# Optimization experiments

Measured on AMD Instinct MI355X. Metric: run time of the kernel, lower is better.

The kernel has to match this reference:

```python
import jax, jax.numpy as jnp
import numpy as np

C = 256  # image_channels == mask_channels == output_channels

def setup_inputs() -> dict:
    key = jax.random.key(0)
    ks = jax.random.split(key, 10)
    B, H, W = 16, 48, 48
    s = 0.02
    return {
        "image_feat": jax.random.normal(ks[0], (B, C, H, W), jnp.float32),
        "mask_feat": jax.random.normal(ks[1], (B, C, H, W), jnp.float32),
        "Wq": jax.random.normal(ks[2], (C, C), jnp.float32) * s,
        "bq": jnp.zeros((C,), jnp.float32),
        "Wk": jax.random.normal(ks[3], (C, C), jnp.float32) * s,
        "bk": jnp.zeros((C,), jnp.float32),
        "Wv": jax.random.normal(ks[4], (C, C), jnp.float32) * s,
        "bv": jnp.zeros((C,), jnp.float32),
        "Wo": jax.random.normal(ks[5], (C, C), jnp.float32) * s,
        "bo": jnp.zeros((C,), jnp.float32),
    }

def reference(image_feat, mask_feat, Wq, bq, Wk, bk, Wv, bv, Wo, bo):
    B, Cc, H, W = image_feat.shape
    N = H * W
    img = image_feat.reshape(B, Cc, N)   # [B, C, N]
    msk = mask_feat.reshape(B, Cc, N)
    # 1x1 convs == per-pixel linear over channels
    q = jnp.einsum('oc,bcn->bon', Wq, msk) + bq[None, :, None]
    k = jnp.einsum('oc,bcn->bon', Wk, img) + bk[None, :, None]
    v = jnp.einsum('oc,bcn->bon', Wv, img) + bv[None, :, None]
    scale = Cc ** (-0.5)
    # attn[b, n, m] = <q[:, n], k[:, m]>
    attn = jnp.einsum('bcn,bcm->bnm', q, k) * scale
    attn = jax.nn.softmax(attn, axis=-1)
    # attended[b, c, n] = sum_m v[b, c, m] * attn[b, n, m]
    av = jnp.einsum('bcm,bnm->bcn', v, attn)
    out = jnp.einsum('oc,bcn->bon', Wo, av) + bo[None, :, None]
    return image_feat + out.reshape(B, Cc, H, W)
```

## Files before the change

### kernel.cpp

```cpp
#include <hip/hip_runtime.h>

#define NBATCH 16
#define CCH 256
#define NTOK 2304

typedef __attribute__((ext_vector_type(8))) short bf16x8;
typedef __attribute__((ext_vector_type(4))) short bf16x4v;
typedef __attribute__((ext_vector_type(4))) float f32x4;

__device__ __forceinline__ short f2bf(float x){
  unsigned u = __builtin_bit_cast(unsigned, x);
  u = u + 0x7FFFu + ((u >> 16) & 1u);
  return (short)(u >> 16);
}
__device__ __forceinline__ float bf2f(short h){
  unsigned u = ((unsigned)(unsigned short)h) << 16;
  return __builtin_bit_cast(float, u);
}

__device__ __forceinline__ void gld_lds16(const short* g, short* l){
  __builtin_amdgcn_global_load_lds((const __attribute__((address_space(1))) void*)g,
                                   (__attribute__((address_space(3))) void*)l, 16, 0, 0);
}

__global__ __launch_bounds__(256) void cw_kernel(const float* __restrict__ Wq, const float* __restrict__ Wk,
                                                 const float* __restrict__ Wv, const float* __restrict__ Wo,
                                                 short* __restrict__ out){
  int idx = blockIdx.x * 256 + threadIdx.x;
  int which = idx >> 14;
  int off = idx & 16383;
  const float* src = which==0 ? Wq : which==1 ? Wk : which==2 ? Wv : Wo;
  float4 v = ((const float4*)src)[off];
  bf16x4v pk = { f2bf(v.x), f2bf(v.y), f2bf(v.z), f2bf(v.w) };
  *(bf16x4v*)(out + ((size_t)which << 16) + ((size_t)off << 2)) = pk;
}

__global__ __launch_bounds__(256) void prep_kernel(const float* __restrict__ img, const float* __restrict__ msk,
                                                   short* __restrict__ imgT, short* __restrict__ mskT){
  int zz = blockIdx.z; int b = zz >> 1; int which = zz & 1;
  const float* src = (which ? msk : img) + (size_t)b * CCH * NTOK;
  short* dst = (which ? mskT : imgT) + (size_t)b * NTOK * CCH;
  int n0 = blockIdx.x * 64, c0 = blockIdx.y * 64;
  __shared__ __align__(16) short tile[64][72];
  int tid = threadIdx.x;
  int r = tid >> 2, g = tid & 3;
  const float* p = src + (size_t)(c0 + r) * NTOK + n0 + 16 * g;
  #pragma unroll
  for (int q4 = 0; q4 < 4; q4++){
    float4 v = *(const float4*)(p + 4 * q4);
    tile[16*g + 4*q4 + 0][r] = f2bf(v.x);
    tile[16*g + 4*q4 + 1][r] = f2bf(v.y);
    tile[16*g + 4*q4 + 2][r] = f2bf(v.z);
    tile[16*g + 4*q4 + 3][r] = f2bf(v.w);
  }
  __syncthreads();
  short* qp = dst + (size_t)(n0 + r) * CCH + c0 + 16 * g;
  *(bf16x8*)qp = *(const bf16x8*)&tile[r][16*g];
  *(bf16x8*)(qp + 8) = *(const bf16x8*)&tile[r][16*g + 8];
}

__device__ __forceinline__ void gemm128(const short* __restrict__ Ablk, const short* __restrict__ Bblk,
                                        short* As, short* Bs, f32x4 (&acc)[4][4]){
  const int tid = threadIdx.x;
  const int l = tid & 63, w = tid >> 6;
  const int l15 = l & 15, lhi = l >> 4;
  const int wi = w >> 1, wj = w & 1;
  const int srow = tid >> 3, scs = tid & 7;
  const f32x4 z4 = {0.f, 0.f, 0.f, 0.f};
  #pragma unroll
  for (int mt = 0; mt < 4; mt++)
    #pragma unroll
    for (int nt = 0; nt < 4; nt++) acc[mt][nt] = z4;

  #pragma unroll 1
  for (int kt = 0; kt < 4; kt++){
    const int k0 = kt * 64;
    bf16x8 ra[4], rb[4];
    #pragma unroll
    for (int p = 0; p < 4; p++){
      const int row = p * 32 + srow;
      ra[p] = *(const bf16x8*)(Ablk + (size_t)row * CCH + k0 + 8 * scs);
      rb[p] = *(const bf16x8*)(Bblk + (size_t)row * CCH + k0 + 8 * scs);
    }
    __syncthreads();
    #pragma unroll
    for (int p = 0; p < 4; p++){
      const int row = p * 32 + srow;
      const int sw = (scs ^ (row & 7)) << 3;
      *(bf16x8*)(As + row * 64 + sw) = ra[p];
      *(bf16x8*)(Bs + row * 64 + sw) = rb[p];
    }
    __syncthreads();
    #pragma unroll
    for (int kk = 0; kk < 2; kk++){
      bf16x8 afr[4], bfr[4];
      #pragma unroll
      for (int mt = 0; mt < 4; mt++){
        const int row = 64 * wi + 16 * mt + l15;
        const int ch = 4 * kk + lhi;
        afr[mt] = *(const bf16x8*)(As + row * 64 + ((ch ^ (row & 7)) << 3));
      }
      #pragma unroll
      for (int nt = 0; nt < 4; nt++){
        const int row = 64 * wj + 16 * nt + l15;
        const int ch = 4 * kk + lhi;
        bfr[nt] = *(const bf16x8*)(Bs + row * 64 + ((ch ^ (row & 7)) << 3));
      }
      #pragma unroll
      for (int mt = 0; mt < 4; mt++)
        #pragma unroll
        for (int nt = 0; nt < 4; nt++)
          acc[mt][nt] = __builtin_amdgcn_mfma_f32_16x16x32_bf16(afr[mt], bfr[nt], acc[mt][nt], 0, 0, 0);
    }
  }
}

__global__ __launch_bounds__(256) void proj_kernel(const short* __restrict__ imgT, const short* __restrict__ mskT,
                                                   const short* __restrict__ Wb,
                                                   const float* __restrict__ bq, const float* __restrict__ bk,
                                                   const float* __restrict__ bv,
                                                   short* __restrict__ Qt, short* __restrict__ Kt,
                                                   short* __restrict__ Vn){
  __shared__ __align__(16) short As[128 * 64];
  __shared__ __align__(16) short Bs[128 * 64];
  const int b = blockIdx.z, which = blockIdx.y, bx = blockIdx.x;
  const size_t nbT = (size_t)b * NTOK * CCH;
  const short* Ablk; const short* Bblk; short* outp; const float* bias;
  int ti, tj, ldout; bool biasRow; float scl;
  if (which == 0){
    ti = bx >> 1; tj = bx & 1;
    Ablk = mskT + nbT + (size_t)ti * 128 * CCH;
    Bblk = Wb + (size_t)tj * 128 * CCH;
    outp = Qt + nbT; bias = bq; ldout = CCH; biasRow = false;
    scl = 0.0625f * 1.44269504088896f;
  } else if (which == 1){
    ti = bx >> 1; tj = bx & 1;
    Ablk = imgT + nbT + (size_t)ti * 128 * CCH;
    Bblk = Wb + 65536 + (size_t)tj * 128 * CCH;
    outp = Kt + nbT; bias = bk; ldout = CCH; biasRow = false; scl = 1.0f;
  } else {
    ti = bx / 18; tj = bx % 18;
    Ablk = Wb + 2 * 65536 + (size_t)ti * 128 * CCH;
    Bblk = imgT + nbT + (size_t)tj * 128 * CCH;
    outp = Vn + nbT; bias = bv; ldout = NTOK; biasRow = true; scl = 1.0f;
  }
  f32x4 acc[4][4];
  gemm128(Ablk, Bblk, As, Bs, acc);
  const int l = threadIdx.x & 63, w = threadIdx.x >> 6;
  const int l15 = l & 15, lhi = l >> 4, wi = w >> 1, wj = w & 1;
  #pragma unroll
  for (int mt = 0; mt < 4; mt++){
    const int i0 = ti * 128 + 64 * wi + 16 * mt + 4 * lhi;
    #pragma unroll
    for (int nt = 0; nt < 4; nt++){
      const int j = tj * 128 + 64 * wj + 16 * nt + l15;
      const float bj = biasRow ? 0.f : bias[j];
      #pragma unroll
      for (int r = 0; r < 4; r++){
        float v = acc[mt][nt][r] + (biasRow ? bias[i0 + r] : bj);
        outp[(size_t)(i0 + r) * ldout + j] = f2bf(v * scl);
      }
    }
  }
}

__global__ __launch_bounds__(256) void attn_kernel(const short* __restrict__ Qt, const short* __restrict__ Kt,
                                                   const short* __restrict__ Vn,
                                                   short* __restrict__ Opart, float* __restrict__ lsumg){
  const int phys = blockIdx.x;
  const int L = (phys & 7) * 144 + (phys >> 3);
  const int b = L / 72;
  const int rem = L % 72;
  const int half = rem / 36;
  const int q0 = (rem % 36) * 64;
  const int t0 = half * 18;
  const int tid = threadIdx.x, w = tid >> 6, l = tid & 63;
  const int l15 = l & 15, lhi = l >> 4;
  const short* Qb = Qt + (size_t)b * NTOK * CCH;
  const short* Kb = Kt + (size_t)b * NTOK * CCH;
  const short* Vb = Vn + (size_t)b * CCH * NTOK;
  __shared__ __align__(16) short Ks[64 * 256];
  __shared__ __align__(16) short P_lds[64 * 64];

  const int st_row = (l >> 5);
  const int st_ch  = (l & 31);

  bf16x8 qf[8];
  {
    const short* qrow = Qb + (size_t)(q0 + 16 * w + l15) * CCH + 8 * lhi;
    #pragma unroll
    for (int kk = 0; kk < 8; kk++) qf[kk] = *(const bf16x8*)(qrow + 32 * kk);
  }
  const f32x4 z4 = {0.f, 0.f, 0.f, 0.f};
  f32x4 oacc[4][4];
  #pragma unroll
  for (int qt = 0; qt < 4; qt++)
    #pragma unroll
    for (int ct = 0; ct < 4; ct++) oacc[qt][ct] = z4;
  float lpart[4] = {0.f, 0.f, 0.f, 0.f};

#define STAGE_K(M0) do { \
    _Pragma("unroll") \
    for (int r = 0; r < 8; r++){ \
      const int slot = 4 * r + w; \
      const int row = 2 * slot + st_row; \
      const int ch = st_ch ^ (row & 7); \
      gld_lds16(Kb + (size_t)((M0) + row) * CCH + (ch << 3), &Ks[slot * 512]); \
    } } while(0)

  STAGE_K(t0 * 64);

  #pragma unroll 1
  for (int t = t0; t < t0 + 18; t++){
    const int m0 = t * 64;
    __syncthreads();

    bf16x8 vfp[8];
    #pragma unroll
    for (int km = 0; km < 2; km++)
      #pragma unroll
      for (int ct = 0; ct < 4; ct++)
        vfp[4 * km + ct] = *(const bf16x8*)(Vb + (size_t)(64 * w + 16 * ct + l15) * NTOK + m0 + 32 * km + 8 * lhi);

    f32x4 sacc[4] = {z4, z4, z4, z4};
    __builtin_amdgcn_s_setprio(1);
    #pragma unroll
    for (int mjb = 0; mjb < 4; mjb++){
      const int row = 16 * mjb + l15;
      const int rsw = row & 7;
      #pragma unroll
      for (int kk = 0; kk < 8; kk++){
        bf16x8 kf = *(const bf16x8*)(Ks + row * 256 + (((4 * kk + lhi) ^ rsw) << 3));
        sacc[mjb] = __builtin_amdgcn_mfma_f32_16x16x32_bf16(qf[kk], kf, sacc[mjb], 0, 0, 0);
      }
    }
    __builtin_amdgcn_s_setprio(0);
    #pragma unroll
    for (int mjb = 0; mjb < 4; mjb++)
      #pragma unroll
      for (int r = 0; r < 4; r++){
        float p = exp2f(sacc[mjb][r]);
        lpart[r] += p;
        const int prow = 16 * w + 4 * lhi + r;
        const int pcol = 16 * mjb + l15;
        P_lds[prow * 64 + ((((pcol >> 3) ^ (prow & 7)) << 3) | (pcol & 7))] = f2bf(p);
      }
    __syncthreads();

    if (t + 1 < t0 + 18) STAGE_K(m0 + 64);

    __builtin_amdgcn_s_setprio(1);
    #pragma unroll
    for (int km = 0; km < 2; km++){
      bf16x8 pf[4];
      #pragma unroll
      for (int qt = 0; qt < 4; qt++){
        const int prow = 16 * qt + l15;
        pf[qt] = *(const bf16x8*)&P_lds[prow * 64 + (((4 * km + lhi) ^ (prow & 7)) << 3)];
      }
      #pragma unroll
      for (int qt = 0; qt < 4; qt++)
        #pragma unroll
        for (int ct = 0; ct < 4; ct++)
          oacc[qt][ct] = __builtin_amdgcn_mfma_f32_16x16x32_bf16(pf[qt], vfp[4 * km + ct], oacc[qt][ct], 0, 0, 0);
    }
    __builtin_amdgcn_s_setprio(0);
  }
#undef STAGE_K

  const size_t hrow = ((size_t)half * NBATCH + b) * NTOK + q0;
  #pragma unroll
  for (int r = 0; r < 4; r++){
    float s = lpart[r];
    s += __shfl_xor(s, 1); s += __shfl_xor(s, 2); s += __shfl_xor(s, 4); s += __shfl_xor(s, 8);
    if (l15 == 0) lsumg[hrow + 16 * w + 4 * lhi + r] = s;
  }
  short* Ob = Opart + hrow * CCH;
  #pragma unroll
  for (int qt = 0; qt < 4; qt++)
    #pragma unroll
    for (int ct = 0; ct < 4; ct++)
      #pragma unroll
      for (int r = 0; r < 4; r++)
        Ob[(size_t)(16 * qt + 4 * lhi + r) * CCH + 64 * w + 16 * ct + l15] = f2bf(oacc[qt][ct][r]);
}

__global__ __launch_bounds__(256) void reduce_kernel(const short* __restrict__ Op, const float* __restrict__ ls,
                                                     short* __restrict__ avT){
  const size_t HSZ = (size_t)NBATCH * NTOK * CCH;
  int idx = blockIdx.x * 256 + threadIdx.x;
  int row = idx >> 5;
  int c0 = (idx & 31) << 3;
  float inv = 1.0f / (ls[row] + ls[NBATCH * NTOK + row]);
  bf16x8 a = *(const bf16x8*)(Op + (size_t)row * CCH + c0);
  bf16x8 c = *(const bf16x8*)(Op + HSZ + (size_t)row * CCH + c0);
  bf16x8 o;
  #pragma unroll
  for (int j = 0; j < 8; j++)
    o[j] = f2bf((bf2f(a[j]) + bf2f(c[j])) * inv);
  *(bf16x8*)(avT + (size_t)row * CCH + c0) = o;
}

__global__ __launch_bounds__(256) void final_kernel(const short* __restrict__ Wb, const short* __restrict__ avT,
                                                    const float* __restrict__ bo, const float* __restrict__ img,
                                                    float* __restrict__ out){
  __shared__ __align__(16) short As[128 * 64];
  __shared__ __align__(16) short Bs[128 * 64];
  const int b = blockIdx.y, bx = blockIdx.x;
  const int ti = bx / 18, tj = bx % 18;
  const short* Ablk = Wb + 3 * 65536 + (size_t)ti * 128 * CCH;
  const short* Bblk = avT + (size_t)b * NTOK * CCH + (size_t)tj * 128 * CCH;
  f32x4 acc[4][4];
  gemm128(Ablk, Bblk, As, Bs, acc);
  const int l = threadIdx.x & 63, w = threadIdx.x >> 6;
  const int l15 = l & 15, lhi = l >> 4, wi = w >> 1, wj = w & 1;
  const float* imgb = img + (size_t)b * CCH * NTOK;
  float* outb = out + (size_t)b * CCH * NTOK;
  #pragma unroll
  for (int mt = 0; mt < 4; mt++){
    const int i0 = ti * 128 + 64 * wi + 16 * mt + 4 * lhi;
    #pragma unroll
    for (int nt = 0; nt < 4; nt++){
      const int j = tj * 128 + 64 * wj + 16 * nt + l15;
      #pragma unroll
      for (int r = 0; r < 4; r++){
        const size_t idx = (size_t)(i0 + r) * NTOK + j;
        outb[idx] = acc[mt][nt][r] + bo[i0 + r] + imgb[idx];
      }
    }
  }
}

extern "C" void kernel_launch(void* const* d_in, const int* in_sizes, int n_in,
                              void* d_out, int out_size, void* d_ws, size_t ws_size,
                              hipStream_t stream) {
  const float* img = (const float*)d_in[0];
  const float* msk = (const float*)d_in[1];
  const float* Wq  = (const float*)d_in[2];
  const float* bq  = (const float*)d_in[3];
  const float* Wk  = (const float*)d_in[4];
  const float* bk  = (const float*)d_in[5];
  const float* Wv  = (const float*)d_in[6];
  const float* bv  = (const float*)d_in[7];
  const float* Wo  = (const float*)d_in[8];
  const float* bo  = (const float*)d_in[9];
  float* out = (float*)d_out;

  short* ws = (short*)d_ws;
  const size_t NE = (size_t)NBATCH * NTOK * CCH;
  short* imgT = ws;
  short* mskT = ws + NE;
  short* Qt   = ws + 2 * NE;
  short* Kt   = ws + 3 * NE;
  short* Vn   = ws + 4 * NE;
  short* Wb   = ws + 5 * NE;
  float* lsumg = (float*)(ws + 5 * NE + 4 * 65536);
  short* avT  = mskT;
  short* Opart = (short*)d_out;

  cw_kernel<<<dim3(256), dim3(256), 0, stream>>>(Wq, Wk, Wv, Wo, Wb);
  prep_kernel<<<dim3(36, 4, 32), dim3(256), 0, stream>>>(img, msk, imgT, mskT);
  proj_kernel<<<dim3(36, 3, 16), dim3(256), 0, stream>>>(imgT, mskT, Wb, bq, bk, bv, Qt, Kt, Vn);
  attn_kernel<<<dim3(1152), dim3(256), 0, stream>>>(Qt, Kt, Vn, Opart, lsumg);
  reduce_kernel<<<dim3(4608), dim3(256), 0, stream>>>(Opart, lsumg, avT);
  final_kernel<<<dim3(36, 16), dim3(256), 0, stream>>>(Wb, avT, bo, img, out);
}
```

Before: 250.2 us.

## Fuse transpose/convert into QKV projection and split-reduce into output GEMM

The separate weight-conversion, input-transpose and projection kernels are merged into one qkv_kernel. It reads fp32 NCHW inputs and weights directly, converts them to bf16 in LDS, and computes a 128-token by 256-channel tile per 512-thread block. The split-attention reduce is folded into the output projection, which normalizes the two partial outputs while staging them into LDS. The Op partials move from the output buffer to workspace. This removes three launches and the bf16 intermediate round trips, at the cost of redundant weight conversion in every block and larger blocks with lower occupancy.

```diff
diff --git a/kernel.cpp b/kernel.cpp
--- a/kernel.cpp
+++ b/kernel.cpp
@@ -23,50 +23,27 @@
                                    (__attribute__((address_space(3))) void*)l, 16, 0, 0);
 }
 
-__global__ __launch_bounds__(256) void cw_kernel(const float* __restrict__ Wq, const float* __restrict__ Wk,
-                                                 const float* __restrict__ Wv, const float* __restrict__ Wo,
-                                                 short* __restrict__ out){
-  int idx = blockIdx.x * 256 + threadIdx.x;
-  int which = idx >> 14;
-  int off = idx & 16383;
-  const float* src = which==0 ? Wq : which==1 ? Wk : which==2 ? Wv : Wo;
-  float4 v = ((const float4*)src)[off];
-  bf16x4v pk = { f2bf(v.x), f2bf(v.y), f2bf(v.z), f2bf(v.w) };
-  *(bf16x4v*)(out + ((size_t)which << 16) + ((size_t)off << 2)) = pk;
-}
-
-__global__ __launch_bounds__(256) void prep_kernel(const float* __restrict__ img, const float* __restrict__ msk,
-                                                   short* __restrict__ imgT, short* __restrict__ mskT){
-  int zz = blockIdx.z; int b = zz >> 1; int which = zz & 1;
-  const float* src = (which ? msk : img) + (size_t)b * CCH * NTOK;
-  short* dst = (which ? mskT : imgT) + (size_t)b * NTOK * CCH;
-  int n0 = blockIdx.x * 64, c0 = blockIdx.y * 64;
-  __shared__ __align__(16) short tile[64][72];
-  int tid = threadIdx.x;
-  int r = tid >> 2, g = tid & 3;
-  const float* p = src + (size_t)(c0 + r) * NTOK + n0 + 16 * g;
-  #pragma unroll
-  for (int q4 = 0; q4 < 4; q4++){
-    float4 v = *(const float4*)(p + 4 * q4);
-    tile[16*g + 4*q4 + 0][r] = f2bf(v.x);
-    tile[16*g + 4*q4 + 1][r] = f2bf(v.y);
-    tile[16*g + 4*q4 + 2][r] = f2bf(v.z);
-    tile[16*g + 4*q4 + 3][r] = f2bf(v.w);
-  }
-  __syncthreads();
-  short* qp = dst + (size_t)(n0 + r) * CCH + c0 + 16 * g;
-  *(bf16x8*)qp = *(const bf16x8*)&tile[r][16*g];
-  *(bf16x8*)(qp + 8) = *(const bf16x8*)&tile[r][16*g + 8];
-}
-
-__device__ __forceinline__ void gemm128(const short* __restrict__ Ablk, const short* __restrict__ Bblk,
-                                        short* As, short* Bs, f32x4 (&acc)[4][4]){
-  const int tid = threadIdx.x;
-  const int l = tid & 63, w = tid >> 6;
+__global__ __launch_bounds__(512, 4) void qkv_kernel(
+    const float* __restrict__ img, const float* __restrict__ msk,
+    const float* __restrict__ Wq, const float* __restrict__ bq,
+    const float* __restrict__ Wk, const float* __restrict__ bk,
+    const float* __restrict__ Wv, const float* __restrict__ bv,
+    short* __restrict__ Qt, short* __restrict__ Kt, short* __restrict__ Vn){
+  __shared__ __align__(16) short XL[128 * 72];
+  __shared__ __align__(16) short WL[256 * 64];
+  const int ti = blockIdx.x, which = blockIdx.y, b = blockIdx.z;
+  const int n0 = ti * 128;
+  const int t = threadIdx.x, wv = t >> 6, l = t & 63;
   const int l15 = l & 15, lhi = l >> 4;
-  const int wi = w >> 1, wj = w & 1;
-  const int srow = tid >> 3, scs = tid & 7;
+  const float* X = (which == 0 ? msk : img) + (size_t)b * CCH * NTOK;
+  const float* W = which == 0 ? Wq : (which == 1 ? Wk : Wv);
+  const float* bias = which == 0 ? bq : (which == 1 ? bk : bv);
+  const int sc = t >> 3, sg = t & 7;
+  const int xch = sc >> 3, xg = sc & 7;
+  const int so = t >> 1, sh = t & 1;
+
   const f32x4 z4 = {0.f, 0.f, 0.f, 0.f};
+  f32x4 acc[4][4];
   #pragma unroll
   for (int mt = 0; mt < 4; mt++)
     #pragma unroll
@@ -74,91 +51,104 @@
 
   #pragma unroll 1
   for (int kt = 0; kt < 4; kt++){
-    const int k0 = kt * 64;
-    bf16x8 ra[4], rb[4];
-    #pragma unroll
-    for (int p = 0; p < 4; p++){
-      const int row = p * 32 + srow;
-      ra[p] = *(const bf16x8*)(Ablk + (size_t)row * CCH + k0 + 8 * scs);
-      rb[p] = *(const bf16x8*)(Bblk + (size_t)row * CCH + k0 + 8 * scs);
-    }
-    __syncthreads();
-    #pragma unroll
-    for (int p = 0; p < 4; p++){
-      const int row = p * 32 + srow;
-      const int sw = (scs ^ (row & 7)) << 3;
-      *(bf16x8*)(As + row * 64 + sw) = ra[p];
-      *(bf16x8*)(Bs + row * 64 + sw) = rb[p];
-    }
-    __syncthreads();
-    #pragma unroll
-    for (int kk = 0; kk < 2; kk++){
-      bf16x8 afr[4], bfr[4];
-      #pragma unroll
-      for (int mt = 0; mt < 4; mt++){
-        const int row = 64 * wi + 16 * mt + l15;
-        const int ch = 4 * kk + lhi;
-        afr[mt] = *(const bf16x8*)(As + row * 64 + ((ch ^ (row & 7)) << 3));
-      }
+    const int c0 = kt * 64;
+    float4 xv[4];
+    #pragma unroll
+    for (int q = 0; q < 4; q++)
+      xv[q] = *(const float4*)(X + (size_t)(c0 + sc) * NTOK + n0 + 16 * sg + 4 * q);
+    float4 wreg[8];
+    #pragma unroll
+    for (int q = 0; q < 8; q++)
+      wreg[q] = *(const float4*)(W + (size_t)so * CCH + c0 + 32 * sh + 4 * q);
+    __syncthreads();
+    #pragma unroll
+    for (int q = 0; q < 4; q++){
+      const float vals[4] = {xv[q].x, xv[q].y, xv[q].z, xv[q].w};
+      #pragma unroll
+      for (int e = 0; e < 4; e++){
+        const int n = 16 * sg + 4 * q + e;
+        XL[n * 72 + (((xch ^ sg) << 3) | xg)] = f2bf(vals[e]);
+      }
+    }
+    #pragma unroll
+    for (int q = 0; q < 8; q++){
+      const int cl = 32 * sh + 4 * q;
+      bf16x4v pk = { f2bf(wreg[q].x), f2bf(wreg[q].y), f2bf(wreg[q].z), f2bf(wreg[q].w) };
+      *(bf16x4v*)&WL[so * 64 + ((((cl >> 3) ^ (so & 7)) << 3) | (cl & 7))] = pk;
+    }
+    __syncthreads();
+    if (which < 2){
+      const int wi = wv >> 2, wj = wv & 3;
+      #pragma unroll
+      for (int kk = 0; kk < 2; kk++){
+        bf16x8 af[4], bf_[4];
+        #pragma unroll
+        for (int mt = 0; mt < 4; mt++){
+          const int n = 64 * wi + 16 * mt + l15;
+          af[mt] = *(const bf16x8*)&XL[n * 72 + (((4 * kk + lhi) ^ ((n >> 4) & 7)) << 3)];
+        }
+        #pragma unroll
+        for (int nt = 0; nt < 4; nt++){
+          const int o = 64 * wj + 16 * nt + l15;
+          bf_[nt] = *(const bf16x8*)&WL[o * 64 + (((4 * kk + lhi) ^ (o & 7)) << 3)];
+        }
+        #pragma unroll
+        for (int mt = 0; mt < 4; mt++)
+          #pragma unroll
+          for (int nt = 0; nt < 4; nt++)
+            acc[mt][nt] = __builtin_amdgcn_mfma_f32_16x16x32_bf16(af[mt], bf_[nt], acc[mt][nt], 0, 0, 0);
+      }
+    } else {
+      const int wi = wv & 3, wj = wv >> 2;
+      #pragma unroll
+      for (int kk = 0; kk < 2; kk++){
+        bf16x8 af[4], bf_[4];
+        #pragma unroll
+        for (int mt = 0; mt < 4; mt++){
+          const int o = 64 * wi + 16 * mt + l15;
+          af[mt] = *(const bf16x8*)&WL[o * 64 + (((4 * kk + lhi) ^ (o & 7)) << 3)];
+        }
+        #pragma unroll
+        for (int nt = 0; nt < 4; nt++){
+          const int n = 64 * wj + 16 * nt + l15;
+          bf_[nt] = *(const bf16x8*)&XL[n * 72 + (((4 * kk + lhi) ^ ((n >> 4) & 7)) << 3)];
+        }
+        #pragma unroll
+        for (int mt = 0; mt < 4; mt++)
+          #pragma unroll
+          for (int nt = 0; nt < 4; nt++)
+            acc[mt][nt] = __builtin_amdgcn_mfma_f32_16x16x32_bf16(af[mt], bf_[nt], acc[mt][nt], 0, 0, 0);
+      }
+    }
+  }
+  if (which < 2){
+    short* outp = (which == 0 ? Qt : Kt) + (size_t)b * NTOK * CCH;
+    const float scl = which == 0 ? 0.0625f * 1.44269504088896f : 1.0f;
+    const int wi = wv >> 2, wj = wv & 3;
+    #pragma unroll
+    for (int mt = 0; mt < 4; mt++){
+      const int nb = n0 + 64 * wi + 16 * mt + 4 * lhi;
       #pragma unroll
       for (int nt = 0; nt < 4; nt++){
-        const int row = 64 * wj + 16 * nt + l15;
-        const int ch = 4 * kk + lhi;
-        bfr[nt] = *(const bf16x8*)(Bs + row * 64 + ((ch ^ (row & 7)) << 3));
-      }
-      #pragma unroll
-      for (int mt = 0; mt < 4; mt++)
-        #pragma unroll
-        for (int nt = 0; nt < 4; nt++)
-          acc[mt][nt] = __builtin_amdgcn_mfma_f32_16x16x32_bf16(afr[mt], bfr[nt], acc[mt][nt], 0, 0, 0);
-    }
-  }
-}
-
-__global__ __launch_bounds__(256) void proj_kernel(const short* __restrict__ imgT, const short* __restrict__ mskT,
-                                                   const short* __restrict__ Wb,
-                                                   const float* __restrict__ bq, const float* __restrict__ bk,
-                                                   const float* __restrict__ bv,
-                                                   short* __restrict__ Qt, short* __restrict__ Kt,
-                                                   short* __restrict__ Vn){
-  __shared__ __align__(16) short As[128 * 64];
-  __shared__ __align__(16) short Bs[128 * 64];
-  const int b = blockIdx.z, which = blockIdx.y, bx = blockIdx.x;
-  const size_t nbT = (size_t)b * NTOK * CCH;
-  const short* Ablk; const short* Bblk; short* outp; const float* bias;
-  int ti, tj, ldout; bool biasRow; float scl;
-  if (which == 0){
-    ti = bx >> 1; tj = bx & 1;
-    Ablk = mskT + nbT + (size_t)ti * 128 * CCH;
-    Bblk = Wb + (size_t)tj * 128 * CCH;
-    outp = Qt + nbT; bias = bq; ldout = CCH; biasRow = false;
-    scl = 0.0625f * 1.44269504088896f;
-  } else if (which == 1){
-    ti = bx >> 1; tj = bx & 1;
-    Ablk = imgT + nbT + (size_t)ti * 128 * CCH;
-    Bblk = Wb + 65536 + (size_t)tj * 128 * CCH;
-    outp = Kt + nbT; bias = bk; ldout = CCH; biasRow = false; scl = 1.0f;
+        const int o = 64 * wj + 16 * nt + l15;
+        const float bj = bias[o];
+        #pragma unroll
+        for (int r = 0; r < 4; r++)
+          outp[(size_t)(nb + r) * CCH + o] = f2bf((acc[mt][nt][r] + bj) * scl);
+      }
+    }
   } else {
-    ti = bx / 18; tj = bx % 18;
-    Ablk = Wb + 2 * 65536 + (size_t)ti * 128 * CCH;
-    Bblk = imgT + nbT + (size_t)tj * 128 * CCH;
-    outp = Vn + nbT; bias = bv; ldout = NTOK; biasRow = true; scl = 1.0f;
-  }
-  f32x4 acc[4][4];
-  gemm128(Ablk, Bblk, As, Bs, acc);
-  const int l = threadIdx.x & 63, w = threadIdx.x >> 6;
-  const int l15 = l & 15, lhi = l >> 4, wi = w >> 1, wj = w & 1;
-  #pragma unroll
-  for (int mt = 0; mt < 4; mt++){
-    const int i0 = ti * 128 + 64 * wi + 16 * mt + 4 * lhi;
-    #pragma unroll
-    for (int nt = 0; nt < 4; nt++){
-      const int j = tj * 128 + 64 * wj + 16 * nt + l15;
-      const float bj = biasRow ? 0.f : bias[j];
-      #pragma unroll
-      for (int r = 0; r < 4; r++){
-        float v = acc[mt][nt][r] + (biasRow ? bias[i0 + r] : bj);
-        outp[(size_t)(i0 + r) * ldout + j] = f2bf(v * scl);
+    short* outp = Vn + (size_t)b * CCH * NTOK;
+    const int wi = wv & 3, wj = wv >> 2;
+    #pragma unroll
+    for (int mt = 0; mt < 4; mt++){
+      const int ob = 64 * wi + 16 * mt + 4 * lhi;
+      #pragma unroll
+      for (int nt = 0; nt < 4; nt++){
+        const int ng = n0 + 64 * wj + 16 * nt + l15;
+        #pragma unroll
+        for (int r = 0; r < 4; r++)
+          outp[(size_t)(ob + r) * NTOK + ng] = f2bf(acc[mt][nt][r] + bias[ob + r]);
       }
     }
   }
@@ -285,47 +275,94 @@
         Ob[(size_t)(16 * qt + 4 * lhi + r) * CCH + 64 * w + 16 * ct + l15] = f2bf(oacc[qt][ct][r]);
 }
 
-__global__ __launch_bounds__(256) void reduce_kernel(const short* __restrict__ Op, const float* __restrict__ ls,
-                                                     short* __restrict__ avT){
-  const size_t HSZ = (size_t)NBATCH * NTOK * CCH;
-  int idx = blockIdx.x * 256 + threadIdx.x;
-  int row = idx >> 5;
-  int c0 = (idx & 31) << 3;
-  float inv = 1.0f / (ls[row] + ls[NBATCH * NTOK + row]);
-  bf16x8 a = *(const bf16x8*)(Op + (size_t)row * CCH + c0);
-  bf16x8 c = *(const bf16x8*)(Op + HSZ + (size_t)row * CCH + c0);
-  bf16x8 o;
-  #pragma unroll
-  for (int j = 0; j < 8; j++)
-    o[j] = f2bf((bf2f(a[j]) + bf2f(c[j])) * inv);
-  *(bf16x8*)(avT + (size_t)row * CCH + c0) = o;
-}
-
-__global__ __launch_bounds__(256) void final_kernel(const short* __restrict__ Wb, const short* __restrict__ avT,
-                                                    const float* __restrict__ bo, const float* __restrict__ img,
-                                                    float* __restrict__ out){
-  __shared__ __align__(16) short As[128 * 64];
-  __shared__ __align__(16) short Bs[128 * 64];
-  const int b = blockIdx.y, bx = blockIdx.x;
-  const int ti = bx / 18, tj = bx % 18;
-  const short* Ablk = Wb + 3 * 65536 + (size_t)ti * 128 * CCH;
-  const short* Bblk = avT + (size_t)b * NTOK * CCH + (size_t)tj * 128 * CCH;
+__global__ __launch_bounds__(512, 4) void final_kernel(
+    const float* __restrict__ Wo, const float* __restrict__ bo,
+    const short* __restrict__ Op, const float* __restrict__ ls,
+    const float* __restrict__ img, float* __restrict__ out){
+  __shared__ __align__(16) short XL[128 * 72];
+  __shared__ __align__(16) short WL[256 * 64];
+  const int ti = blockIdx.x, b = blockIdx.y;
+  const int n0 = ti * 128;
+  const int t = threadIdx.x, wv = t >> 6, l = t & 63;
+  const int l15 = l & 15, lhi = l >> 4;
+  const int sn = t >> 2, sj = t & 3;
+  const int so = t >> 1, sh = t & 1;
+  const size_t HS = (size_t)NBATCH * NTOK * CCH;
+  const size_t row = (size_t)b * NTOK + n0 + sn;
+  const float inv = 1.0f / (ls[row] + ls[(size_t)NBATCH * NTOK + row]);
+
+  const f32x4 z4 = {0.f, 0.f, 0.f, 0.f};
   f32x4 acc[4][4];
-  gemm128(Ablk, Bblk, As, Bs, acc);
-  const int l = threadIdx.x & 63, w = threadIdx.x >> 6;
-  const int l15 = l & 15, lhi = l >> 4, wi = w >> 1, wj = w & 1;
+  #pragma unroll
+  for (int mt = 0; mt < 4; mt++)
+    #pragma unroll
+    for (int nt = 0; nt < 4; nt++) acc[mt][nt] = z4;
+
+  #pragma unroll 1
+  for (int kt = 0; kt < 4; kt++){
+    const int c0 = kt * 64;
+    bf16x8 a0[2], a1[2];
+    #pragma unroll
+    for (int j = 0; j < 2; j++){
+      const int c = c0 + (2 * sj + j) * 8;
+      a0[j] = *(const bf16x8*)(Op + row * CCH + c);
+      a1[j] = *(const bf16x8*)(Op + HS + row * CCH + c);
+    }
+    float4 wreg[8];
+    #pragma unroll
+    for (int q = 0; q < 8; q++)
+      wreg[q] = *(const float4*)(Wo + (size_t)so * CCH + c0 + 32 * sh + 4 * q);
+    __syncthreads();
+    #pragma unroll
+    for (int j = 0; j < 2; j++){
+      const int ch = 2 * sj + j;
+      bf16x8 cb;
+      #pragma unroll
+      for (int e = 0; e < 8; e++)
+        cb[e] = f2bf((bf2f(a0[j][e]) + bf2f(a1[j][e])) * inv);
+      *(bf16x8*)&XL[sn * 72 + ((ch ^ ((sn >> 4) & 7)) << 3)] = cb;
+    }
+    #pragma unroll
+    for (int q = 0; q < 8; q++){
+      const int cl = 32 * sh + 4 * q;
+      bf16x4v pk = { f2bf(wreg[q].x), f2bf(wreg[q].y), f2bf(wreg[q].z), f2bf(wreg[q].w) };
+      *(bf16x4v*)&WL[so * 64 + ((((cl >> 3) ^ (so & 7)) << 3) | (cl & 7))] = pk;
+    }
+    __syncthreads();
+    const int wi = wv & 3, wj = wv >> 2;
+    #pragma unroll
+    for (int kk = 0; kk < 2; kk++){
+      bf16x8 af[4], bf_[4];
+      #pragma unroll
+      for (int mt = 0; mt < 4; mt++){
+        const int o = 64 * wi + 16 * mt + l15;
+        af[mt] = *(const bf16x8*)&WL[o * 64 + (((4 * kk + lhi) ^ (o & 7)) << 3)];
+      }
+      #pragma unroll
+      for (int nt = 0; nt < 4; nt++){
+        const int n = 64 * wj + 16 * nt + l15;
+        bf_[nt] = *(const bf16x8*)&XL[n * 72 + (((4 * kk + lhi) ^ ((n >> 4) & 7)) << 3)];
+      }
+      #pragma unroll
+      for (int mt = 0; mt < 4; mt++)
+        #pragma unroll
+        for (int nt = 0; nt < 4; nt++)
+          acc[mt][nt] = __builtin_amdgcn_mfma_f32_16x16x32_bf16(af[mt], bf_[nt], acc[mt][nt], 0, 0, 0);
+    }
+  }
+  const int wi = wv & 3, wj = wv >> 2;
   const float* imgb = img + (size_t)b * CCH * NTOK;
   float* outb = out + (size_t)b * CCH * NTOK;
   #pragma unroll
   for (int mt = 0; mt < 4; mt++){
-    const int i0 = ti * 128 + 64 * wi + 16 * mt + 4 * lhi;
+    const int ob = 64 * wi + 16 * mt + 4 * lhi;
     #pragma unroll
     for (int nt = 0; nt < 4; nt++){
-      const int j = tj * 128 + 64 * wj + 16 * nt + l15;
+      const int ng = n0 + 64 * wj + 16 * nt + l15;
       #pragma unroll
       for (int r = 0; r < 4; r++){
-        const size_t idx = (size_t)(i0 + r) * NTOK + j;
-        outb[idx] = acc[mt][nt][r] + bo[i0 + r] + imgb[idx];
+        const size_t idx = (size_t)(ob + r) * NTOK + ng;
+        outb[idx] = acc[mt][nt][r] + bo[ob + r] + imgb[idx];
       }
     }
   }
@@ -348,20 +385,13 @@
 
   short* ws = (short*)d_ws;
   const size_t NE = (size_t)NBATCH * NTOK * CCH;
-  short* imgT = ws;
-  short* mskT = ws + NE;
-  short* Qt   = ws + 2 * NE;
-  short* Kt   = ws + 3 * NE;
-  short* Vn   = ws + 4 * NE;
-  short* Wb   = ws + 5 * NE;
-  float* lsumg = (float*)(ws + 5 * NE + 4 * 65536);
-  short* avT  = mskT;
-  short* Opart = (short*)d_out;
-
-  cw_kernel<<<dim3(256), dim3(256), 0, stream>>>(Wq, Wk, Wv, Wo, Wb);
-  prep_kernel<<<dim3(36, 4, 32), dim3(256), 0, stream>>>(img, msk, imgT, mskT);
-  proj_kernel<<<dim3(36, 3, 16), dim3(256), 0, stream>>>(imgT, mskT, Wb, bq, bk, bv, Qt, Kt, Vn);
-  attn_kernel<<<dim3(1152), dim3(256), 0, stream>>>(Qt, Kt, Vn, Opart, lsumg);
-  reduce_kernel<<<dim3(4608), dim3(256), 0, stream>>>(Opart, lsumg, avT);
-  final_kernel<<<dim3(36, 16), dim3(256), 0, stream>>>(Wb, avT, bo, img, out);
-}
+  short* Qt = ws;
+  short* Kt = ws + NE;
+  short* Vn = ws + 2 * NE;
+  short* Op = ws + 3 * NE;
+  float* lsumg = (float*)(ws + 5 * NE);
+
+  qkv_kernel<<<dim3(18, 3, 16), dim3(512), 0, stream>>>(img, msk, Wq, bq, Wk, bk, Wv, bv, Qt, Kt, Vn);
+  attn_kernel<<<dim3(1152), dim3(256), 0, stream>>>(Qt, Kt, Vn, Op, lsumg);
+  final_kernel<<<dim3(18, 16), dim3(512), 0, stream>>>(Wo, bo, Op, lsumg, img, out);
+}
```

Result: slower. 314.3 us (+25.6%).

## Fuse split-K reduce and normalization into output projection GEMM

Applied to the files above, without the earlier changes.

Removes the separate reduce kernel: the output-projection kernel now loads both attention partial outputs, sums them, divides by the combined softmax denominators, and writes the bf16 result straight into swizzled LDS as the GEMM B operand. Wo is converted from fp32 in the kernel, and each 512-thread block covers all 256 output channels for 128 tokens. This saves a kernel launch and a full bf16 write/read round trip of the attended tensor. The cost is less overlap (synchronous loads with no double buffering) and only 288 blocks, and the partials now go to workspace aliasing imgT instead of the output buffer.

```diff
diff --git a/kernel.cpp b/kernel.cpp
--- a/kernel.cpp
+++ b/kernel.cpp
@@ -285,47 +285,94 @@
         Ob[(size_t)(16 * qt + 4 * lhi + r) * CCH + 64 * w + 16 * ct + l15] = f2bf(oacc[qt][ct][r]);
 }
 
-__global__ __launch_bounds__(256) void reduce_kernel(const short* __restrict__ Op, const float* __restrict__ ls,
-                                                     short* __restrict__ avT){
-  const size_t HSZ = (size_t)NBATCH * NTOK * CCH;
-  int idx = blockIdx.x * 256 + threadIdx.x;
-  int row = idx >> 5;
-  int c0 = (idx & 31) << 3;
-  float inv = 1.0f / (ls[row] + ls[NBATCH * NTOK + row]);
-  bf16x8 a = *(const bf16x8*)(Op + (size_t)row * CCH + c0);
-  bf16x8 c = *(const bf16x8*)(Op + HSZ + (size_t)row * CCH + c0);
-  bf16x8 o;
-  #pragma unroll
-  for (int j = 0; j < 8; j++)
-    o[j] = f2bf((bf2f(a[j]) + bf2f(c[j])) * inv);
-  *(bf16x8*)(avT + (size_t)row * CCH + c0) = o;
-}
-
-__global__ __launch_bounds__(256) void final_kernel(const short* __restrict__ Wb, const short* __restrict__ avT,
-                                                    const float* __restrict__ bo, const float* __restrict__ img,
-                                                    float* __restrict__ out){
-  __shared__ __align__(16) short As[128 * 64];
-  __shared__ __align__(16) short Bs[128 * 64];
-  const int b = blockIdx.y, bx = blockIdx.x;
-  const int ti = bx / 18, tj = bx % 18;
-  const short* Ablk = Wb + 3 * 65536 + (size_t)ti * 128 * CCH;
-  const short* Bblk = avT + (size_t)b * NTOK * CCH + (size_t)tj * 128 * CCH;
+__global__ __launch_bounds__(512, 4) void final_kernel(
+    const float* __restrict__ Wo, const float* __restrict__ bo,
+    const short* __restrict__ Op, const float* __restrict__ ls,
+    const float* __restrict__ img, float* __restrict__ out){
+  __shared__ __align__(16) short XL[128 * 72];
+  __shared__ __align__(16) short WL[256 * 64];
+  const int ti = blockIdx.x, b = blockIdx.y;
+  const int n0 = ti * 128;
+  const int t = threadIdx.x, wv = t >> 6, l = t & 63;
+  const int l15 = l & 15, lhi = l >> 4;
+  const int sn = t >> 2, sj = t & 3;
+  const int so = t >> 1, sh = t & 1;
+  const size_t HS = (size_t)NBATCH * NTOK * CCH;
+  const size_t row = (size_t)b * NTOK + n0 + sn;
+  const float inv = 1.0f / (ls[row] + ls[(size_t)NBATCH * NTOK + row]);
+
+  const f32x4 z4 = {0.f, 0.f, 0.f, 0.f};
   f32x4 acc[4][4];
-  gemm128(Ablk, Bblk, As, Bs, acc);
-  const int l = threadIdx.x & 63, w = threadIdx.x >> 6;
-  const int l15 = l & 15, lhi = l >> 4, wi = w >> 1, wj = w & 1;
+  #pragma unroll
+  for (int mt = 0; mt < 4; mt++)
+    #pragma unroll
+    for (int nt = 0; nt < 4; nt++) acc[mt][nt] = z4;
+
+  #pragma unroll 1
+  for (int kt = 0; kt < 4; kt++){
+    const int c0 = kt * 64;
+    bf16x8 a0[2], a1[2];
+    #pragma unroll
+    for (int j = 0; j < 2; j++){
+      const int c = c0 + (2 * sj + j) * 8;
+      a0[j] = *(const bf16x8*)(Op + row * CCH + c);
+      a1[j] = *(const bf16x8*)(Op + HS + row * CCH + c);
+    }
+    float4 wreg[8];
+    #pragma unroll
+    for (int q = 0; q < 8; q++)
+      wreg[q] = *(const float4*)(Wo + (size_t)so * CCH + c0 + 32 * sh + 4 * q);
+    __syncthreads();
+    #pragma unroll
+    for (int j = 0; j < 2; j++){
+      const int ch = 2 * sj + j;
+      bf16x8 cb;
+      #pragma unroll
+      for (int e = 0; e < 8; e++)
+        cb[e] = f2bf((bf2f(a0[j][e]) + bf2f(a1[j][e])) * inv);
+      *(bf16x8*)&XL[sn * 72 + ((ch ^ ((sn >> 4) & 7)) << 3)] = cb;
+    }
+    #pragma unroll
+    for (int q = 0; q < 8; q++){
+      const int cl = 32 * sh + 4 * q;
+      bf16x4v pk = { f2bf(wreg[q].x), f2bf(wreg[q].y), f2bf(wreg[q].z), f2bf(wreg[q].w) };
+      *(bf16x4v*)&WL[so * 64 + ((((cl >> 3) ^ (so & 7)) << 3) | (cl & 7))] = pk;
+    }
+    __syncthreads();
+    const int wi = wv & 3, wj = wv >> 2;
+    #pragma unroll
+    for (int kk = 0; kk < 2; kk++){
+      bf16x8 af[4], bf_[4];
+      #pragma unroll
+      for (int mt = 0; mt < 4; mt++){
+        const int o = 64 * wi + 16 * mt + l15;
+        af[mt] = *(const bf16x8*)&WL[o * 64 + (((4 * kk + lhi) ^ (o & 7)) << 3)];
+      }
+      #pragma unroll
+      for (int nt = 0; nt < 4; nt++){
+        const int n = 64 * wj + 16 * nt + l15;
+        bf_[nt] = *(const bf16x8*)&XL[n * 72 + (((4 * kk + lhi) ^ ((n >> 4) & 7)) << 3)];
+      }
+      #pragma unroll
+      for (int mt = 0; mt < 4; mt++)
+        #pragma unroll
+        for (int nt = 0; nt < 4; nt++)
+          acc[mt][nt] = __builtin_amdgcn_mfma_f32_16x16x32_bf16(af[mt], bf_[nt], acc[mt][nt], 0, 0, 0);
+    }
+  }
+  const int wi = wv & 3, wj = wv >> 2;
   const float* imgb = img + (size_t)b * CCH * NTOK;
   float* outb = out + (size_t)b * CCH * NTOK;
   #pragma unroll
   for (int mt = 0; mt < 4; mt++){
-    const int i0 = ti * 128 + 64 * wi + 16 * mt + 4 * lhi;
+    const int ob = 64 * wi + 16 * mt + 4 * lhi;
     #pragma unroll
     for (int nt = 0; nt < 4; nt++){
-      const int j = tj * 128 + 64 * wj + 16 * nt + l15;
+      const int ng = n0 + 64 * wj + 16 * nt + l15;
       #pragma unroll
       for (int r = 0; r < 4; r++){
-        const size_t idx = (size_t)(i0 + r) * NTOK + j;
-        outb[idx] = acc[mt][nt][r] + bo[i0 + r] + imgb[idx];
+        const size_t idx = (size_t)(ob + r) * NTOK + ng;
+        outb[idx] = acc[mt][nt][r] + bo[ob + r] + imgb[idx];
       }
     }
   }
@@ -355,13 +402,11 @@
   short* Vn   = ws + 4 * NE;
   short* Wb   = ws + 5 * NE;
   float* lsumg = (float*)(ws + 5 * NE + 4 * 65536);
-  short* avT  = mskT;
-  short* Opart = (short*)d_out;
+  short* Op   = ws;
 
   cw_kernel<<<dim3(256), dim3(256), 0, stream>>>(Wq, Wk, Wv, Wo, Wb);
   prep_kernel<<<dim3(36, 4, 32), dim3(256), 0, stream>>>(img, msk, imgT, mskT);
   proj_kernel<<<dim3(36, 3, 16), dim3(256), 0, stream>>>(imgT, mskT, Wb, bq, bk, bv, Qt, Kt, Vn);
-  attn_kernel<<<dim3(1152), dim3(256), 0, stream>>>(Qt, Kt, Vn, Opart, lsumg);
-  reduce_kernel<<<dim3(4608), dim3(256), 0, stream>>>(Opart, lsumg, avT);
-  final_kernel<<<dim3(36, 16), dim3(256), 0, stream>>>(Wb, avT, bo, img, out);
-}
+  attn_kernel<<<dim3(1152), dim3(256), 0, stream>>>(Qt, Kt, Vn, Op, lsumg);
+  final_kernel<<<dim3(18, 16), dim3(512), 0, stream>>>(Wo, bo, Op, lsumg, img, out);
+}
```

New measurement: 255.7 us. 1.02x slower.
